# Kernel tuning notes

Measured on AMD Instinct MI355X. Metric: run time of the kernel, lower is better.

The kernel has to match this reference:

```python
import jax, jax.numpy as jnp
import numpy as np

B, S, D_MODEL, K_CH, OUT = 16, 8192, 256, 256, 256


def setup_inputs() -> dict:
    key = jax.random.key(0)
    ks = jax.random.split(key, 9)
    s = lambda fan_in: 1.0 / np.sqrt(fan_in)
    return {
        "query": jax.random.normal(ks[0], (B, D_MODEL), dtype=jnp.float32),
        "key": jax.random.normal(ks[1], (B, S, K_CH), dtype=jnp.float32),
        "value": jax.random.normal(ks[2], (B, S, K_CH), dtype=jnp.float32),
        "Wq": jax.random.uniform(ks[3], (D_MODEL, OUT), jnp.float32, -s(D_MODEL), s(D_MODEL)),
        "bq": jax.random.uniform(ks[4], (OUT,), jnp.float32, -s(D_MODEL), s(D_MODEL)),
        "Wk": jax.random.uniform(ks[5], (K_CH, OUT), jnp.float32, -s(K_CH), s(K_CH)),
        "bk": jax.random.uniform(ks[6], (OUT,), jnp.float32, -s(K_CH), s(K_CH)),
        "Wv": jax.random.uniform(ks[7], (K_CH, OUT), jnp.float32, -s(K_CH), s(K_CH)),
        "bv": jax.random.uniform(ks[8], (OUT,), jnp.float32, -s(K_CH), s(K_CH)),
    }


def reference(query, key, value, Wq, bq, Wk, bk, Wv, bv):
    # q is a single vector per batch; the torch module expands it to S identical
    # rows, making every output row identical. We compute one row and broadcast
    # -- mathematically identical, O(S*d) instead of O(S^2*d).
    q = query @ Wq + bq                      # [B, OUT]
    k = jnp.einsum("bsc,co->bso", key, Wk) + bk    # [B, S, OUT]
    v = jnp.einsum("bsc,co->bso", value, Wv) + bv  # [B, S, OUT]
    scale = 1.0 / jnp.sqrt(jnp.float32(q.shape[-1]))
    scores = jnp.einsum("bo,bso->bs", q, k) * scale  # [B, S]
    w = jax.nn.softmax(scores, axis=-1)              # [B, S]
    ctx = jnp.einsum("bs,bso->bo", w, v)             # [B, OUT]
    seq_len = k.shape[1]
    return jnp.broadcast_to(ctx[:, None, :], (ctx.shape[0], seq_len, ctx.shape[1]))
```

## Files before the change

### kernel.cpp

```cpp
#include <hip/hip_runtime.h>

typedef float f4 __attribute__((ext_vector_type(4)));

constexpr int Bn = 16;
constexpr int Sn = 8192;
constexpr int Dn = 256;
constexpr float kScale = 0.0625f;
constexpr int NCHUNK = 64;
constexpr int CHUNK  = Sn / NCHUNK;

constexpr int R_OFF    = 0;
constexpr int C_OFF    = R_OFF + Bn * Dn;
constexpr int M_OFF    = C_OFF + 64;
constexpr int SUM_OFF  = M_OFF + Bn * NCHUNK;
constexpr int PART_OFF = SUM_OFF + Bn * NCHUNK;

__global__ __launch_bounds__(256) void k_qrc(
    const float* __restrict__ query, const float* __restrict__ Wq,
    const float* __restrict__ bq, const float* __restrict__ Wk,
    const float* __restrict__ bk, float* __restrict__ ws) {
  int b = blockIdx.x, t = threadIdx.x;
  __shared__ float qs[Dn];
  __shared__ float qh[Dn];
  __shared__ float red[256];
  qs[t] = query[b * Dn + t];
  __syncthreads();
  float acc = bq[t];
  #pragma unroll 32
  for (int d = 0; d < Dn; ++d) acc += qs[d] * Wq[d * Dn + t];
  qh[t] = acc;
  __syncthreads();
  float racc = 0.f;
  const f4* wkrow = (const f4*)(Wk + (size_t)t * Dn);
  const f4* qh4 = (const f4*)qh;
  #pragma unroll 16
  for (int o4 = 0; o4 < Dn / 4; ++o4) {
    f4 wv = wkrow[o4];
    f4 qv = qh4[o4];
    racc += wv.x * qv.x + wv.y * qv.y + wv.z * qv.z + wv.w * qv.w;
  }
  ws[R_OFF + b * Dn + t] = racc;
  red[t] = qh[t] * bk[t];
  __syncthreads();
  for (int off = 128; off; off >>= 1) {
    if (t < off) red[t] += red[t + off];
    __syncthreads();
  }
  if (t == 0) ws[C_OFF + b] = red[0];
}

__global__ __launch_bounds__(256) void k_fused(
    const float* __restrict__ key, const float* __restrict__ value,
    float* __restrict__ ws) {
  int blk = blockIdx.x;
  int b = blk >> 6;
  int chunk = blk & 63;
  int s0 = chunk * CHUNK;
  int t = threadIdx.x, lane = t & 63, wv = t >> 6;
  __shared__ float sc[CHUNK];
  __shared__ float wsh[CHUNK];
  __shared__ float red[4][Dn];

  f4 rv = ((const f4*)(ws + R_OFF + b * Dn))[lane];
  float cb = ws[C_OFF + b];
  const f4* kp = (const f4*)(key + ((size_t)b * Sn + s0) * Dn);
  const f4* vp = (const f4*)(value + ((size_t)b * Sn + s0) * Dn);

  #pragma unroll 4
  for (int i = 0; i < CHUNK / 4; ++i) {
    int sl = wv + 4 * i;
    f4 kv = __builtin_nontemporal_load(&kp[(size_t)sl * 64 + lane]);
    float dot = kv.x * rv.x + kv.y * rv.y + kv.z * rv.z + kv.w * rv.w;
    #pragma unroll
    for (int off = 32; off; off >>= 1) dot += __shfl_xor(dot, off, 64);
    if (lane == 0) sc[sl] = (dot + cb) * kScale;
  }
  __syncthreads();

  float m = -1e30f;
  #pragma unroll 8
  for (int i = 0; i < CHUNK; ++i) m = fmaxf(m, sc[i]);
  if (t < CHUNK) wsh[t] = __expf(sc[t] - m);
  __syncthreads();

  f4 vacc = {0.f, 0.f, 0.f, 0.f};
  #pragma unroll 4
  for (int i = 0; i < CHUNK / 4; ++i) {
    int sl = wv + 4 * i;
    f4 v = __builtin_nontemporal_load(&vp[(size_t)sl * 64 + lane]);
    float w = wsh[sl];
    vacc.x += w * v.x; vacc.y += w * v.y; vacc.z += w * v.z; vacc.w += w * v.w;
  }
  red[wv][lane * 4 + 0] = vacc.x;
  red[wv][lane * 4 + 1] = vacc.y;
  red[wv][lane * 4 + 2] = vacc.z;
  red[wv][lane * 4 + 3] = vacc.w;
  __syncthreads();
  float part = red[0][t] + red[1][t] + red[2][t] + red[3][t];
  ws[PART_OFF + ((size_t)b * NCHUNK + chunk) * Dn + t] = part;
  if (t == 0) {
    float ssum = 0.f;
    #pragma unroll 8
    for (int i = 0; i < CHUNK; ++i) ssum += wsh[i];
    ws[M_OFF + b * NCHUNK + chunk] = m;
    ws[SUM_OFF + b * NCHUNK + chunk] = ssum;
  }
}

__global__ __launch_bounds__(256) void k_out(
    const float* __restrict__ Wv, const float* __restrict__ bv,
    const float* __restrict__ ws, float* __restrict__ out) {
  int blk = blockIdx.x;
  int b = blk >> 6;
  int chunk = blk & 63;
  int s0 = chunk * CHUNK;
  int t = threadIdx.x, lane = t & 63, wv = t >> 6;

  __shared__ float msh[NCHUNK];
  __shared__ float e[NCHUNK];
  __shared__ float ush[Dn];
  __shared__ float ctx[Dn];

  if (t < NCHUNK) msh[t] = ws[M_OFF + b * NCHUNK + t];
  __syncthreads();
  float gm = -1e30f;
  #pragma unroll 16
  for (int c = 0; c < NCHUNK; ++c) gm = fmaxf(gm, msh[c]);
  if (t < NCHUNK) e[t] = __expf(msh[t] - gm);
  __syncthreads();
  float denom = 0.f;
  #pragma unroll 16
  for (int c = 0; c < NCHUNK; ++c) denom += ws[SUM_OFF + b * NCHUNK + c] * e[c];
  float u = 0.f;
  #pragma unroll 16
  for (int c = 0; c < NCHUNK; ++c)
    u += ws[PART_OFF + ((size_t)b * NCHUNK + c) * Dn + t] * e[c];
  ush[t] = u / denom;
  __syncthreads();
  float acc = bv[t];
  #pragma unroll 16
  for (int o = 0; o < Dn; ++o) acc += ush[o] * Wv[o * Dn + t];
  ctx[t] = acc;
  __syncthreads();

  f4 val = ((const f4*)ctx)[lane];
  f4* op = (f4*)(out + ((size_t)b * Sn + s0) * Dn);
  #pragma unroll 8
  for (int it = 0; it < CHUNK / 4; ++it) {
    int sl = wv + 4 * it;
    __builtin_nontemporal_store(val, &op[(size_t)sl * 64 + lane]);
  }
}

extern "C" void kernel_launch(void* const* d_in, const int* in_sizes, int n_in,
                              void* d_out, int out_size, void* d_ws, size_t ws_size,
                              hipStream_t stream) {
  const float* query = (const float*)d_in[0];
  const float* key   = (const float*)d_in[1];
  const float* value = (const float*)d_in[2];
  const float* Wq    = (const float*)d_in[3];
  const float* bq    = (const float*)d_in[4];
  const float* Wk    = (const float*)d_in[5];
  const float* bk    = (const float*)d_in[6];
  const float* Wv    = (const float*)d_in[7];
  const float* bv    = (const float*)d_in[8];
  float* out = (float*)d_out;
  float* ws  = (float*)d_ws;

  hipLaunchKernelGGL(k_qrc,   dim3(Bn),          dim3(256), 0, stream,
                     query, Wq, bq, Wk, bk, ws);
  hipLaunchKernelGGL(k_fused, dim3(Bn * NCHUNK), dim3(256), 0, stream,
                     key, value, ws);
  hipLaunchKernelGGL(k_out,   dim3(Bn * NCHUNK), dim3(256), 0, stream,
                     Wv, bv, ws, out);
}
```

Baseline: 102.6 us.

## Use online softmax per wave to stream key and value in one pass

The chunk kernel now loads key and value rows together and keeps a per-wave online softmax (running max, sum, rescaled value accumulator). This removes the shared-memory score buffer, the serial max and sum loops, and one block barrier. It also makes the two streams overlap. The chunk count doubles to 128 to give more blocks, while the output kernel keeps 64 blocks per batch and caches the partial sums in shared memory. The cost is more exp calls and branchy rescaling per row, and twice as many partials for the combine step to read.

```diff
diff --git a/kernel.cpp b/kernel.cpp
--- a/kernel.cpp
+++ b/kernel.cpp
@@ -6,8 +6,9 @@
 constexpr int Sn = 8192;
 constexpr int Dn = 256;
 constexpr float kScale = 0.0625f;
-constexpr int NCHUNK = 64;
+constexpr int NCHUNK = 128;
 constexpr int CHUNK  = Sn / NCHUNK;
+constexpr int OROWS  = 128;
 
 constexpr int R_OFF    = 0;
 constexpr int C_OFF    = R_OFF + Bn * Dn;
@@ -53,57 +54,59 @@
     const float* __restrict__ key, const float* __restrict__ value,
     float* __restrict__ ws) {
   int blk = blockIdx.x;
-  int b = blk >> 6;
-  int chunk = blk & 63;
+  int b = blk >> 7;
+  int chunk = blk & 127;
   int s0 = chunk * CHUNK;
   int t = threadIdx.x, lane = t & 63, wv = t >> 6;
-  __shared__ float sc[CHUNK];
-  __shared__ float wsh[CHUNK];
-  __shared__ float red[4][Dn];
+
+  __shared__ float wm[4], wsum[4];
+  __shared__ f4 wva[4][64];
 
   f4 rv = ((const f4*)(ws + R_OFF + b * Dn))[lane];
   float cb = ws[C_OFF + b];
   const f4* kp = (const f4*)(key + ((size_t)b * Sn + s0) * Dn);
   const f4* vp = (const f4*)(value + ((size_t)b * Sn + s0) * Dn);
 
+  float m = -1e30f, sum = 0.f;
+  f4 vacc = {0.f, 0.f, 0.f, 0.f};
+
   #pragma unroll 4
   for (int i = 0; i < CHUNK / 4; ++i) {
     int sl = wv + 4 * i;
     f4 kv = __builtin_nontemporal_load(&kp[(size_t)sl * 64 + lane]);
+    f4 vv = __builtin_nontemporal_load(&vp[(size_t)sl * 64 + lane]);
     float dot = kv.x * rv.x + kv.y * rv.y + kv.z * rv.z + kv.w * rv.w;
     #pragma unroll
     for (int off = 32; off; off >>= 1) dot += __shfl_xor(dot, off, 64);
-    if (lane == 0) sc[sl] = (dot + cb) * kScale;
+    float s = (dot + cb) * kScale;
+    if (s > m) {
+      float sc = __expf(m - s);
+      sum *= sc;
+      vacc *= sc;
+      m = s;
+    }
+    float w = __expf(s - m);
+    sum += w;
+    vacc += w * vv;
   }
+
+  if (lane == 0) { wm[wv] = m; wsum[wv] = sum; }
+  wva[wv][lane] = vacc;
   __syncthreads();
 
-  float m = -1e30f;
-  #pragma unroll 8
-  for (int i = 0; i < CHUNK; ++i) m = fmaxf(m, sc[i]);
-  if (t < CHUNK) wsh[t] = __expf(sc[t] - m);
-  __syncthreads();
-
-  f4 vacc = {0.f, 0.f, 0.f, 0.f};
-  #pragma unroll 4
-  for (int i = 0; i < CHUNK / 4; ++i) {
-    int sl = wv + 4 * i;
-    f4 v = __builtin_nontemporal_load(&vp[(size_t)sl * 64 + lane]);
-    float w = wsh[sl];
-    vacc.x += w * v.x; vacc.y += w * v.y; vacc.z += w * v.z; vacc.w += w * v.w;
-  }
-  red[wv][lane * 4 + 0] = vacc.x;
-  red[wv][lane * 4 + 1] = vacc.y;
-  red[wv][lane * 4 + 2] = vacc.z;
-  red[wv][lane * 4 + 3] = vacc.w;
-  __syncthreads();
-  float part = red[0][t] + red[1][t] + red[2][t] + red[3][t];
+  float gm = fmaxf(fmaxf(wm[0], wm[1]), fmaxf(wm[2], wm[3]));
+  float e0 = __expf(wm[0] - gm), e1 = __expf(wm[1] - gm);
+  float e2 = __expf(wm[2] - gm), e3 = __expf(wm[3] - gm);
+  const float* v0 = (const float*)&wva[0][0];
+  const float* v1 = (const float*)&wva[1][0];
+  const float* v2 = (const float*)&wva[2][0];
+  const float* v3 = (const float*)&wva[3][0];
+  float part = v0[t] * e0 + v1[t] * e1 + v2[t] * e2 + v3[t] * e3;
   ws[PART_OFF + ((size_t)b * NCHUNK + chunk) * Dn + t] = part;
   if (t == 0) {
-    float ssum = 0.f;
-    #pragma unroll 8
-    for (int i = 0; i < CHUNK; ++i) ssum += wsh[i];
-    ws[M_OFF + b * NCHUNK + chunk] = m;
-    ws[SUM_OFF + b * NCHUNK + chunk] = ssum;
+    ws[M_OFF + b * NCHUNK + chunk] = gm;
+    ws[SUM_OFF + b * NCHUNK + chunk] =
+        wsum[0] * e0 + wsum[1] * e1 + wsum[2] * e2 + wsum[3] * e3;
   }
 }
 
@@ -112,16 +115,18 @@
     const float* __restrict__ ws, float* __restrict__ out) {
   int blk = blockIdx.x;
   int b = blk >> 6;
-  int chunk = blk & 63;
-  int s0 = chunk * CHUNK;
+  int oc = blk & 63;
+  int s0 = oc * OROWS;
   int t = threadIdx.x, lane = t & 63, wv = t >> 6;
 
   __shared__ float msh[NCHUNK];
+  __shared__ float ssh[NCHUNK];
   __shared__ float e[NCHUNK];
   __shared__ float ush[Dn];
   __shared__ float ctx[Dn];
 
   if (t < NCHUNK) msh[t] = ws[M_OFF + b * NCHUNK + t];
+  else            ssh[t - NCHUNK] = ws[SUM_OFF + b * NCHUNK + (t - NCHUNK)];
   __syncthreads();
   float gm = -1e30f;
   #pragma unroll 16
@@ -130,7 +135,7 @@
   __syncthreads();
   float denom = 0.f;
   #pragma unroll 16
-  for (int c = 0; c < NCHUNK; ++c) denom += ws[SUM_OFF + b * NCHUNK + c] * e[c];
+  for (int c = 0; c < NCHUNK; ++c) denom += ssh[c] * e[c];
   float u = 0.f;
   #pragma unroll 16
   for (int c = 0; c < NCHUNK; ++c)
@@ -146,7 +151,7 @@
   f4 val = ((const f4*)ctx)[lane];
   f4* op = (f4*)(out + ((size_t)b * Sn + s0) * Dn);
   #pragma unroll 8
-  for (int it = 0; it < CHUNK / 4; ++it) {
+  for (int it = 0; it < OROWS / 4; ++it) {
     int sl = wv + 4 * it;
     __builtin_nontemporal_store(val, &op[(size_t)sl * 64 + lane]);
   }
@@ -171,6 +176,6 @@
                      query, Wq, bq, Wk, bk, ws);
   hipLaunchKernelGGL(k_fused, dim3(Bn * NCHUNK), dim3(256), 0, stream,
                      key, value, ws);
-  hipLaunchKernelGGL(k_out,   dim3(Bn * NCHUNK), dim3(256), 0, stream,
+  hipLaunchKernelGGL(k_out,   dim3(Bn * 64),     dim3(256), 0, stream,
                      Wv, bv, ws, out);
 }
```

Measured after the change: 100.2 us. 2.4% less time.
